# Performance work log

Measured on AMD Instinct MI355X. Metric: run time of the kernel, lower is better.

## Reference

```python
import jax, jax.numpy as jnp
import numpy as np

B, L, D, H, E, M, P = 2, 512, 768, 12, 32, 4, 256
EMB, BS, MAP, C = 768, 64, 256, 97


def setup_inputs() -> dict:
    key = jax.random.key(0)
    ks = jax.random.split(key, 16)
    w = lambda k, s: (0.02 * jax.random.normal(k, s, jnp.float32))
    seq = jax.random.normal(ks[0], (B, L, D), jnp.float32)
    attn = jax.random.uniform(ks[1], (B, H, L, L), jnp.float32)
    entity_pos = jax.random.randint(ks[2], (B, E, M), 0, L - 2)
    # distinct (h, t) entity pairs per document -> unique mention-pair scatter slots
    grid = jnp.stack(jnp.meshgrid(jnp.arange(E), jnp.arange(E), indexing='ij'), -1).reshape(-1, 2)
    hts = jnp.stack([grid[jax.random.permutation(jax.random.fold_in(ks[3], b), E * E)[:P]] for b in range(B)], 0)
    mention_idx = jnp.broadcast_to(jnp.arange(E * M).reshape(E, M), (B, E, M))
    return {
        'seq': seq, 'attn': attn,
        'entity_pos': entity_pos, 'hts': hts, 'mention_idx': mention_idx,
        'W_head': w(ks[4], (2 * D, EMB)), 'b_head': jnp.zeros((EMB,), jnp.float32),
        'W_tail': w(ks[5], (2 * D, EMB)), 'b_tail': jnp.zeros((EMB,), jnp.float32),
        'W_rel': w(ks[6], (EMB * BS, C)), 'b_rel': jnp.zeros((C,), jnp.float32),
        'W_fh': w(ks[7], (D, EMB)), 'W_ft': w(ks[8], (D, EMB)), 'b_f': jnp.zeros((EMB,), jnp.float32),
        'W_unet': w(ks[9], (EMB, C)), 'b_unet': jnp.zeros((C,), jnp.float32),
        'W_mlp': w(ks[10], (EMB, C)), 'b_mlp': jnp.zeros((C,), jnp.float32),
        'W_bil': w(ks[11], (3 * C, C)), 'b_bil': jnp.zeros((C,), jnp.float32),
    }


def reference(seq, attn, entity_pos, hts, mention_idx,
              W_head, b_head, W_tail, b_tail, W_rel, b_rel,
              W_fh, W_ft, b_f, W_unet, b_unet, W_mlp, b_mlp, W_bil, b_bil):
    pos = entity_pos + 1                                 # bert offset
    b3 = jnp.arange(B)[:, None, None]
    ment_emb = seq[b3, pos]                              # [B,E,M,D] mention gather
    ment_att = attn[b3, :, pos]                          # [B,E,M,H,L]
    ent_emb = jax.nn.logsumexp(ment_emb, axis=2)         # [B,E,D] logsumexp pool
    ent_att = ment_att.mean(axis=2)                      # [B,E,H,L]
    b2 = jnp.arange(B)[:, None]
    h_idx, t_idx = hts[..., 0], hts[..., 1]
    hs, ts = ent_emb[b2, h_idx], ent_emb[b2, t_idx]      # [B,P,D]
    ha, ta = ent_att[b2, h_idx], ent_att[b2, t_idx]      # [B,P,H,L]
    ht_att = (ha * ta).mean(2)                           # [B,P,L]
    ht_att = ht_att / (ht_att.sum(-1, keepdims=True) + 1e-5)
    rs = jnp.einsum('bld,bpl->bpd', seq, ht_att)         # localized context
    N = B * P
    hz = jnp.tanh(jnp.concatenate([hs, rs], -1).reshape(N, 2 * D) @ W_head + b_head)
    tz = jnp.tanh(jnp.concatenate([ts, rs], -1).reshape(N, 2 * D) @ W_tail + b_tail)
    bl = (hz.reshape(N, EMB // BS, BS, 1) * tz.reshape(N, EMB // BS, 1, BS)).reshape(N, EMB * BS)
    r1 = bl @ W_rel + b_rel                              # [N,C]
    # mention-pair dense map scatter (map_rss)
    ment_flat = ment_emb.reshape(B, E * M, D)
    mh = mention_idx[b2, h_idx]                          # [B,P,M]
    mt = mention_idx[b2, t_idx]
    mh2 = jnp.broadcast_to(mh[:, :, :, None], (B, P, M, M))
    mt2 = jnp.broadcast_to(mt[:, :, None, :], (B, P, M, M))
    b4 = jnp.broadcast_to(jnp.arange(B)[:, None, None, None], (B, P, M, M))
    eh = ment_flat[b4, mh2]                              # [B,P,M,M,D]
    et = ment_flat[b4, mt2]
    feat = eh @ W_fh + et @ W_ft + b_f                   # fused Linear(cat(h,t))
    mp = jnp.zeros((B, MAP, MAP, EMB), seq.dtype).at[b4, mh2, mt2].set(feat)
    enc2 = jnp.tanh(mp @ W_unet + b_unet)                # UNet-channel surrogate
    enc3 = jax.nn.gelu(mp @ W_mlp + b_mlp)               # MLP-channel surrogate
    r2 = jax.nn.logsumexp(enc2[b4, mh2, mt2], axis=(2, 3)).reshape(N, C)
    r3 = jax.nn.logsumexp(enc3[b4, mh2, mt2], axis=(2, 3)).reshape(N, C)
    return jnp.concatenate([r1, r2, r3], -1) @ W_bil + b_bil
```

## Files before the change

### kernel.cpp

```cpp
#include <hip/hip_runtime.h>
#include <hip/hip_bf16.h>

#define B_  2
#define L_  512
#define D_  768
#define H_  12
#define E_  32
#define M_  4
#define P_  256
#define EMB_ 768
#define BS_ 64
#define C_  97
#define N_  (B_*P_)

#define KTOT_    49152
#define CPAD_    112
#define KSPLIT_  48
#define KCHUNK_  (KTOT_/KSPLIT_)
#define PSTR_    128
#define TILE_    (CPAD_*64)

typedef __hip_bfloat16 bf16;
typedef __attribute__((ext_vector_type(8))) short bf16x8;
typedef __attribute__((ext_vector_type(4))) float f32x4;
typedef __attribute__((ext_vector_type(8))) float f32x8;

__device__ inline float ldIn(const void* p, long idx, int isbf) {
    return isbf ? (float)((const bf16*)p)[idx] : ((const float*)p)[idx];
}

__device__ inline unsigned short f2bf(float f) {
    bf16 h = (bf16)f;
    return *(unsigned short*)&h;
}

__device__ inline float bf2f(unsigned short u) {
    bf16 h = *(bf16*)&u;
    return (float)h;
}

__global__ void dtype_detect(const void* __restrict__ seq, int* __restrict__ flag,
                             float* __restrict__ c23) {
    __shared__ int cnt;
    if (threadIdx.x == 0) cnt = 0;
    if (threadIdx.x < 2*C_) c23[threadIdx.x] = 0.f;
    __syncthreads();
    const unsigned short* u = (const unsigned short*)seq;
    int bad = 0;
    for (int i = threadIdx.x; i < 1024; i += 256) {
        unsigned short e = (u[i] >> 7) & 0xFF;
        if (e >= 140) bad++;
    }
    atomicAdd(&cnt, bad);
    __syncthreads();
    if (threadIdx.x == 0) flag[0] = (cnt < 16) ? 1 : 0;
}

struct PrepArgs {
    const void* src[8];
    long off[8];
    int K[8];
    int Ncols[8];
    int Npad[8];
    unsigned short* dst[8];
    const void* W_bil;  float* W_bilF;
    const void* b_f; const void* W_unet; const void* b_unet;
    const void* W_mlp; const void* b_mlp; float* c23;
    const void* W_rel; unsigned short* WBt;
};

union PrepSm {
    float T[32][65];
    unsigned short TW[CPAD_][72];
};

__global__ void prep_kernel(PrepArgs a, const int* __restrict__ dtf) {
    int isbf = dtf[0];
    int z = blockIdx.z;
    __shared__ PrepSm sm;
    int tid = threadIdx.x;
    if (z == 0) {
        int lin = blockIdx.y*48 + blockIdx.x;
        if (lin >= 96) return;
        int c = tid;
        if (c >= C_) return;
        float s2 = 0.f, s3 = 0.f;
        int d0 = lin*8;
        for (int i = 0; i < 8; i++) {
            int d = d0 + i;
            float bf = ldIn(a.b_f, d, isbf);
            s2 += bf * ldIn(a.W_unet, (long)d*C_ + c, isbf);
            s3 += bf * ldIn(a.W_mlp,  (long)d*C_ + c, isbf);
        }
        if (lin == 0) {
            s2 += ldIn(a.b_unet, c, isbf);
            s3 += ldIn(a.b_mlp,  c, isbf);
        }
        atomicAdd(&a.c23[c], s2);
        atomicAdd(&a.c23[C_ + c], s3);
    } else if (z == 1) {
        int lin = blockIdx.y*48 + blockIdx.x;
        if (lin >= KTOT_/64) return;
        int k0 = lin * 64;
        for (int idx = tid; idx < 64*97; idx += 256) {
            int kk = idx / 97, c = idx % 97;
            sm.TW[c][kk] = f2bf(ldIn(a.W_rel, (long)(k0+kk)*C_ + c, isbf));
        }
        for (int idx = tid; idx < 15*64; idx += 256) {
            sm.TW[97 + (idx>>6)][idx & 63] = 0;
        }
        __syncthreads();
        unsigned short* tb = a.WBt + (long)lin*TILE_;
        for (int t = 0; t < 4; t++) {
            int idx = tid + t*256;
            if (idx < 896) {
                int c = idx >> 3, kc = idx & 7;
                *(uint4*)(tb + idx*8) = *(uint4*)&sm.TW[c][kc*8];
            }
        }
    } else if (z <= 9) {
        int j = z - 2;
        int K = a.K[j], Ncols = a.Ncols[j], Npad = a.Npad[j];
        int k0 = blockIdx.x*32, n0 = blockIdx.y*64;
        if (k0 >= K || n0 >= Npad) return;
        const void* src = a.src[j];
        long off = a.off[j];
        unsigned short* dst = a.dst[j];
        int c64 = tid & 63, r4 = tid >> 6;
        for (int p = 0; p < 8; p++) {
            int r = r4 + p*4;
            int n = n0 + c64;
            sm.T[r][c64] = (n < Ncols) ? ldIn(src, off + (long)(k0+r)*Ncols + n, isbf) : 0.f;
        }
        __syncthreads();
        int cc = tid & 31, n8 = tid >> 5;
        for (int p = 0; p < 8; p++) {
            int nn = n8 + p*8;
            dst[(long)(n0+nn)*K + k0 + cc] = f2bf(sm.T[cc][nn]);
        }
    } else {
        int lin = blockIdx.y*48 + blockIdx.x;
        int idx = lin*256 + tid;
        if (idx < 291*C_) a.W_bilF[idx] = ldIn(a.W_bil, idx, isbf);
    }
}

__global__ void gather_kernel(const void* __restrict__ seq, const void* __restrict__ attn,
                              const int* __restrict__ entity_pos,
                              unsigned short* __restrict__ mentb, float* __restrict__ ent_emb,
                              float* __restrict__ ent_att, const int* __restrict__ dtf) {
    int isbf = dtf[0];
    if (blockIdx.x < 768) {
        int beh = blockIdx.x;
        int h = beh % H_;
        int be = beh / H_;
        int b = be >> 5;
        int pos[M_];
        for (int m = 0; m < M_; m++) pos[m] = entity_pos[be*M_+m] + 1;
        for (int l = threadIdx.x; l < L_; l += 256) {
            float s = 0.f;
            for (int m = 0; m < M_; m++)
                s += ldIn(attn, (((long)(b*H_ + h))*L_ + pos[m])*L_ + l, isbf);
            ent_att[(long)beh*L_ + l] = 0.25f * s;
        }
    } else {
        int be = blockIdx.x - 768;
        int b = be >> 5;
        int pos[M_];
        for (int m = 0; m < M_; m++) pos[m] = entity_pos[be*M_+m] + 1;
        for (int d = threadIdx.x; d < D_; d += 256) {
            float x[M_];
            for (int m = 0; m < M_; m++) {
                x[m] = ldIn(seq, ((long)b*L_ + pos[m])*D_ + d, isbf);
                mentb[((long)be*M_ + m)*D_ + d] = f2bf(x[m]);
            }
            float mx = fmaxf(fmaxf(x[0],x[1]), fmaxf(x[2],x[3]));
            float s = expf(x[0]-mx)+expf(x[1]-mx)+expf(x[2]-mx)+expf(x[3]-mx);
            ent_emb[(long)be*D_ + d] = mx + logf(s);
        }
    }
}

__global__ void htatt_kernel(const float* __restrict__ ent_att, const int* __restrict__ hts,
                             unsigned short* __restrict__ htb) {
    int bp = blockIdx.x;
    int b = bp >> 8;
    int h_e = hts[bp*2+0], t_e = hts[bp*2+1];
    const float* ea_h = ent_att + (long)((b*E_ + h_e)*H_)*L_;
    const float* ea_t = ent_att + (long)((b*E_ + t_e)*H_)*L_;
    __shared__ float red[256];
    float v[2];
    for (int t = 0; t < 2; t++) {
        int l = threadIdx.x + t*256;
        float s = 0.f;
        for (int h = 0; h < H_; h++) s += ea_h[h*L_+l] * ea_t[h*L_+l];
        v[t] = s * (1.0f/H_);
    }
    red[threadIdx.x] = v[0] + v[1];
    __syncthreads();
    for (int off = 128; off > 0; off >>= 1) {
        if (threadIdx.x < off) red[threadIdx.x] += red[threadIdx.x+off];
        __syncthreads();
    }
    float inv = 1.0f / (red[0] + 1e-5f);
    for (int t = 0; t < 2; t++) {
        int l = threadIdx.x + t*256;
        htb[(long)bp*L_ + l] = f2bf(v[t] * inv);
    }
}

__global__ void catb_kernel(const float* __restrict__ ent_emb, const float* __restrict__ rs,
                            const int* __restrict__ hts,
                            unsigned short* __restrict__ hcatb, unsigned short* __restrict__ tcatb) {
    int n = blockIdx.x;
    int b = n >> 8;
    int h_e = hts[n*2+0], t_e = hts[n*2+1];
    const float* eh = ent_emb + (long)(b*E_ + h_e)*D_;
    const float* et = ent_emb + (long)(b*E_ + t_e)*D_;
    const float* r  = rs + (long)n*D_;
    for (int k = threadIdx.x; k < D_; k += 256) {
        hcatb[(long)n*1536 + k] = f2bf(eh[k]);
        tcatb[(long)n*1536 + k] = f2bf(et[k]);
        unsigned short rb = f2bf(r[k]);
        hcatb[(long)n*1536 + 768 + k] = rb;
        tcatb[(long)n*1536 + 768 + k] = rb;
    }
}

struct MfmaJob {
    const unsigned short* A[4];
    const unsigned short* Bt[4];
    const void* bias[4];
    void* C[4];
    int K[4];
    int ldc[4];
    int act[4];
    int obf[4];
};

__global__ void mfma_nt2_kernel(MfmaJob args, const int* __restrict__ dtf) {
    int z = blockIdx.z;
    const unsigned short* A  = args.A[z];
    const unsigned short* Bt = args.Bt[z];
    const void* bias = args.bias[z];
    void* C = args.C[z];
    int K = args.K[z], ldc = args.ldc[z], act = args.act[z], obf = args.obf[z];
    __shared__ unsigned short Al[2][32][72];
    __shared__ unsigned short Btl[2][32][72];
    int m0 = blockIdx.x*32, n0 = blockIdx.y*32;
    int tid = threadIdx.x, wave = tid>>6, lane = tid&63;
    int lm = lane&15, lq = lane>>4;
    int rowg = wave>>1, cgrp = wave&1;
    int rr = tid >> 3;
    int kc = (tid & 7) * 8;
    uint4 ra, rb;

    ra = *(const uint4*)(A  + (long)(m0+rr)*K + kc);
    rb = *(const uint4*)(Bt + (long)(n0+rr)*K + kc);
    *(uint4*)&Al[0][rr][kc]  = ra;
    *(uint4*)&Btl[0][rr][kc] = rb;

    int nst = K >> 6;
    f32x4 acc = {};
    for (int ks = 0; ks < nst; ks++) {
        __syncthreads();
        if (ks+1 < nst) {
            int k0 = (ks+1) << 6;
            ra = *(const uint4*)(A  + (long)(m0+rr)*K + k0 + kc);
            rb = *(const uint4*)(Bt + (long)(n0+rr)*K + k0 + kc);
        }
        int cb = ks & 1;
        #pragma unroll
        for (int half = 0; half < 2; half++) {
            bf16x8 af  = *(bf16x8*)&Al[cb][rowg*16+lm][half*32+lq*8];
            bf16x8 bfr = *(bf16x8*)&Btl[cb][cgrp*16+lm][half*32+lq*8];
            acc = __builtin_amdgcn_mfma_f32_16x16x32_bf16(af, bfr, acc, 0, 0, 0);
        }
        if (ks+1 < nst) {
            int nb = (ks+1) & 1;
            *(uint4*)&Al[nb][rr][kc]  = ra;
            *(uint4*)&Btl[nb][rr][kc] = rb;
        }
    }
    int isbf = dtf[0];
    int n = n0 + cgrp*16 + lm;
    float bia = bias ? ldIn(bias, n, isbf) : 0.f;
    #pragma unroll
    for (int r = 0; r < 4; r++) {
        int m = m0 + rowg*16 + lq*4 + r;
        float v = acc[r] + bia;
        if (act == 1) v = tanhf(v);
        if (obf) ((unsigned short*)C)[(long)m*ldc + n] = f2bf(v);
        else     ((float*)C)[(long)m*ldc + n] = v;
    }
}

__global__ __launch_bounds__(512, 4)
void r1_mfma_kernel(const float* __restrict__ hz, const float* __restrict__ tz,
                    const unsigned short* __restrict__ WBt,
                    float* __restrict__ partial) {
    __shared__ unsigned short Btl[2][CPAD_][72];
    __shared__ float hzL[64][17];
    int kz = blockIdx.x;
    int nb0 = blockIdx.y * 64;
    int gk0 = kz * (KCHUNK_/64);
    int gi0 = kz * 16;
    int g0 = (kz * KCHUNK_) >> 12;
    int tid = threadIdx.x;
    int wave = tid >> 6, lane = tid & 63;
    int lm = lane & 15, lq = lane >> 4;
    int rowg = wave >> 1;
    int cgrp = wave & 1;
    int nct = 4 - cgrp;
    int nrow = nb0 + rowg*16 + lm;

    {
        int r = tid >> 3, q = (tid & 7) * 2;
        float2 v = *(const float2*)(hz + (long)(nb0 + r)*EMB_ + gi0 + q);
        hzL[r][q] = v.x; hzL[r][q+1] = v.y;
    }
    f32x8 t0, t1;
    {
        const float* tp = tz + (long)nrow*EMB_ + g0*64;
        float4 x0 = *(const float4*)(tp + lq*8);
        float4 y0 = *(const float4*)(tp + lq*8 + 4);
        float4 x1 = *(const float4*)(tp + 32 + lq*8);
        float4 y1 = *(const float4*)(tp + 32 + lq*8 + 4);
        t0[0]=x0.x; t0[1]=x0.y; t0[2]=x0.z; t0[3]=x0.w;
        t0[4]=y0.x; t0[5]=y0.y; t0[6]=y0.z; t0[7]=y0.w;
        t1[0]=x1.x; t1[1]=x1.y; t1[2]=x1.z; t1[3]=x1.w;
        t1[4]=y1.x; t1[5]=y1.y; t1[6]=y1.z; t1[7]=y1.w;
    }

    {
        const unsigned short* tbp = WBt + (long)gk0*TILE_;
        #pragma unroll
        for (int t = 0; t < 2; t++) {
            int idx = tid + t*512;
            if (idx < 896) {
                *(uint4*)&Btl[0][idx>>3][(idx&7)*8] = *(const uint4*)(tbp + idx*8);
            }
        }
    }

    f32x4 acc[4] = {};
    uint4 rb[2];
    #pragma unroll 2
    for (int ks = 0; ks < KCHUNK_/64; ks++) {
        __syncthreads();
        if (ks+1 < KCHUNK_/64) {
            const unsigned short* tbp = WBt + (long)(gk0+ks+1)*TILE_;
            #pragma unroll
            for (int t = 0; t < 2; t++) {
                int idx = tid + t*512;
                if (idx < 896) {
                    rb[t] = *(const uint4*)(tbp + idx*8);
                }
            }
        }
        int cb = ks & 1;
        bf16x8 bf0[4], bf1[4];
        #pragma unroll
        for (int ct = 0; ct < 4; ct++) {
            if (ct < nct) {
                bf0[ct] = *(bf16x8*)&Btl[cb][(cgrp*4+ct)*16 + lm][lq*8];
                bf1[ct] = *(bf16x8*)&Btl[cb][(cgrp*4+ct)*16 + lm][32 + lq*8];
            }
        }
        float hvk = hzL[rowg*16 + lm][ks];
        unsigned short oa0[8], oa1[8];
        #pragma unroll
        for (int e = 0; e < 8; e++) {
            oa0[e] = f2bf(t0[e] * hvk);
            oa1[e] = f2bf(t1[e] * hvk);
        }
        bf16x8 a0 = *(bf16x8*)oa0;
        bf16x8 a1 = *(bf16x8*)oa1;
        #pragma unroll
        for (int ct = 0; ct < 4; ct++) {
            if (ct < nct) {
                acc[ct] = __builtin_amdgcn_mfma_f32_16x16x32_bf16(a0, bf0[ct], acc[ct], 0, 0, 0);
                acc[ct] = __builtin_amdgcn_mfma_f32_16x16x32_bf16(a1, bf1[ct], acc[ct], 0, 0, 0);
            }
        }
        if (ks+1 < KCHUNK_/64) {
            int nb = (ks+1) & 1;
            #pragma unroll
            for (int t = 0; t < 2; t++) {
                int idx = tid + t*512;
                if (idx < 896) {
                    *(uint4*)&Btl[nb][idx>>3][(idx&7)*8] = rb[t];
                }
            }
        }
    }
    #pragma unroll
    for (int ct = 0; ct < 4; ct++) {
        int c = (cgrp*4 + ct)*16 + lm;
        #pragma unroll
        for (int r = 0; r < 4; r++) {
            int nl = rowg*16 + lq*4 + r;
            partial[((long)(nb0+nl)*KSPLIT_ + kz)*PSTR_ + c] = acc[ct][r];
        }
    }
}

__global__ void r23out_kernel(const float* __restrict__ partial, const void* __restrict__ b_rel,
                              const float* __restrict__ mu, const float* __restrict__ c23,
                              const int* __restrict__ hts, const int* __restrict__ mention_idx,
                              const float* __restrict__ W_bilF, const void* __restrict__ b_bil,
                              void* __restrict__ out, const int* __restrict__ dtf) {
    int bp = blockIdx.x;
    int b = bp >> 8;
    int c = threadIdx.x;
    int isbf = dtf[0];
    __shared__ float row[292];
    if (c < C_) {
        const float* pr = partial + (long)bp*KSPLIT_*PSTR_;
        float r1v = 0.f;
        #pragma unroll 8
        for (int kz = 0; kz < KSPLIT_; kz++)
            r1v += pr[kz*PSTR_ + c];
        r1v += ldIn(b_rel, c, isbf);
        int h_e = hts[bp*2+0], t_e = hts[bp*2+1];
        const float* mu2h = mu;
        const float* mu2t = mu + 32768;
        const float* mu3h = mu + 65536;
        const float* mu3t = mu + 98304;
        float ah2[4], at2[4], ah3[4], at3[4];
        for (int m = 0; m < 4; m++) {
            int emh = mention_idx[(b*E_ + h_e)*M_ + m];
            int emt = mention_idx[(b*E_ + t_e)*M_ + m];
            ah2[m] = mu2h[(long)(b*128 + emh)*128 + c];
            ah3[m] = mu3h[(long)(b*128 + emh)*128 + c];
            at2[m] = mu2t[(long)(b*128 + emt)*128 + c];
            at3[m] = mu3t[(long)(b*128 + emt)*128 + c];
        }
        float c2 = c23[c], c3 = c23[C_ + c];
        float v2[16], v3[16];
        int q = 0;
        for (int i = 0; i < 4; i++) {
            for (int j = 0; j < 4; j++, q++) {
                float x2 = ah2[i] + at2[j] + c2;
                v2[q] = tanhf(x2);
                float x3 = ah3[i] + at3[j] + c3;
                float t = tanhf(0.7978845608028654f * (x3 + 0.044715f*x3*x3*x3));
                v3[q] = 0.5f * x3 * (1.0f + t);
            }
        }
        float m2 = v2[0], m3 = v3[0];
        for (q = 1; q < 16; q++) { m2 = fmaxf(m2, v2[q]); m3 = fmaxf(m3, v3[q]); }
        float s2 = 0.f, s3 = 0.f;
        for (q = 0; q < 16; q++) { s2 += expf(v2[q]-m2); s3 += expf(v3[q]-m3); }
        row[c]        = r1v;
        row[C_ + c]   = m2 + logf(s2);
        row[2*C_ + c] = m3 + logf(s3);
    }
    __syncthreads();
    if (c >= C_) return;
    float a0 = 0.f, a1 = 0.f, a2 = 0.f, a3 = 0.f;
    #pragma unroll 4
    for (int k = 0; k < 288; k += 4) {
        a0 += row[k+0] * W_bilF[(k+0)*C_ + c];
        a1 += row[k+1] * W_bilF[(k+1)*C_ + c];
        a2 += row[k+2] * W_bilF[(k+2)*C_ + c];
        a3 += row[k+3] * W_bilF[(k+3)*C_ + c];
    }
    a0 += row[288] * W_bilF[288*C_ + c];
    a1 += row[289] * W_bilF[289*C_ + c];
    a2 += row[290] * W_bilF[290*C_ + c];
    float v = a0 + a1 + a2 + a3 + ldIn(b_bil, c, isbf);
    if (isbf) ((bf16*)out)[(long)bp*C_ + c] = (bf16)v;
    else      ((float*)out)[(long)bp*C_ + c] = v;
}

extern "C" void kernel_launch(void* const* d_in, const int* in_sizes, int n_in,
                              void* d_out, int out_size, void* d_ws, size_t ws_size,
                              hipStream_t stream) {
    const void* seq        = d_in[0];
    const void* attn       = d_in[1];
    const int*  entity_pos = (const int*)d_in[2];
    const int*  hts        = (const int*)d_in[3];
    const int*  mention_idx= (const int*)d_in[4];
    const void* W_head     = d_in[5];
    const void* b_head     = d_in[6];
    const void* W_tail     = d_in[7];
    const void* b_tail     = d_in[8];
    const void* W_rel      = d_in[9];
    const void* b_rel      = d_in[10];
    const void* W_fh       = d_in[11];
    const void* W_ft       = d_in[12];
    const void* b_f        = d_in[13];
    const void* W_unet     = d_in[14];
    const void* b_unet     = d_in[15];
    const void* W_mlp      = d_in[16];
    const void* b_mlp      = d_in[17];
    const void* W_bil      = d_in[18];
    const void* b_bil      = d_in[19];

    float* w = (float*)d_ws;
    int*   dtf      = (int*)w;
    unsigned short* mentb = (unsigned short*)(w + 64);
    float* ent_emb  = w + 98368;
    float* ent_att  = w + 147520;
    unsigned short* htb = (unsigned short*)(w + 540736);
    float* rs       = w + 671808;
    float* hz       = w + 1065024;
    float* tz       = w + 1458240;
    float* mu       = w + 1851456;
    float* c23      = w + 1982528;
    unsigned short* seqT  = (unsigned short*)(w + 1982784);
    unsigned short* WhT   = (unsigned short*)(w + 2376000);
    unsigned short* WtT   = (unsigned short*)(w + 2965824);
    unsigned short* WfhT  = (unsigned short*)(w + 3555648);
    unsigned short* WftT  = (unsigned short*)(w + 3850560);
    unsigned short* WunetT= (unsigned short*)(w + 4145472);
    unsigned short* WmlpT = (unsigned short*)(w + 4194624);
    unsigned short* Tbh   = (unsigned short*)(w + 4243776);
    unsigned short* Tbt   = (unsigned short*)(w + 4342080);
    unsigned short* hcatb = (unsigned short*)(w + 4440384);
    unsigned short* tcatb = (unsigned short*)(w + 4833600);
    unsigned short* WBt   = (unsigned short*)(w + 5226816);
    float* partial  = w + 7979328;
    float* W_bilF   = w + 11649344;

    dtype_detect<<<1, 256, 0, stream>>>(seq, dtf, c23);
    {
        PrepArgs a = {};
        const void* srcs[8] = {W_head, W_tail, W_fh, W_ft, W_unet, W_mlp, seq, seq};
        long offs[8]   = {0,0,0,0,0,0,0,393216};
        int Ks[8]      = {1536,1536,768,768,768,768,512,512};
        int Ncols8[8]  = {768,768,768,768,97,97,768,768};
        int Npads[8]   = {768,768,768,768,128,128,768,768};
        unsigned short* dsts[8] = {WhT, WtT, WfhT, WftT, WunetT, WmlpT, seqT, seqT+393216};
        for (int z = 0; z < 8; z++) {
            a.src[z]=srcs[z]; a.off[z]=offs[z]; a.K[z]=Ks[z];
            a.Ncols[z]=Ncols8[z]; a.Npad[z]=Npads[z]; a.dst[z]=dsts[z];
        }
        a.W_bil = W_bil; a.W_bilF = W_bilF;
        a.b_f = b_f; a.W_unet = W_unet; a.b_unet = b_unet;
        a.W_mlp = W_mlp; a.b_mlp = b_mlp; a.c23 = c23;
        a.W_rel = W_rel; a.WBt = WBt;
        prep_kernel<<<dim3(48, 16, 11), 256, 0, stream>>>(a, dtf);
    }
    gather_kernel<<<768 + 64, 256, 0, stream>>>(seq, attn, entity_pos, mentb, ent_emb, ent_att, dtf);
    htatt_kernel<<<N_, 256, 0, stream>>>(ent_att, hts, htb);
    {
        MfmaJob ga = {};
        for (int z = 0; z < 2; z++) {
            ga.A[z] = htb + (long)z*256*512; ga.Bt[z] = seqT + (long)z*393216;
            ga.bias[z] = nullptr; ga.C[z] = rs + (long)z*256*768;
            ga.K[z] = 512; ga.ldc[z] = 768; ga.act[z] = 0; ga.obf[z] = 0;
        }
        ga.A[2] = mentb; ga.Bt[2] = WfhT; ga.bias[2] = nullptr; ga.C[2] = Tbh;
        ga.K[2] = 768; ga.ldc[2] = 768; ga.act[2] = 0; ga.obf[2] = 1;
        ga.A[3] = mentb; ga.Bt[3] = WftT; ga.bias[3] = nullptr; ga.C[3] = Tbt;
        ga.K[3] = 768; ga.ldc[3] = 768; ga.act[3] = 0; ga.obf[3] = 1;
        mfma_nt2_kernel<<<dim3(8, 24, 4), 256, 0, stream>>>(ga, dtf);
    }
    catb_kernel<<<N_, 256, 0, stream>>>(ent_emb, rs, hts, hcatb, tcatb);
    {
        MfmaJob ga = {};
        ga.A[0] = hcatb; ga.Bt[0] = WhT; ga.bias[0] = b_head; ga.C[0] = hz;
        ga.A[1] = tcatb; ga.Bt[1] = WtT; ga.bias[1] = b_tail; ga.C[1] = tz;
        for (int z = 0; z < 2; z++) { ga.K[z] = 1536; ga.ldc[z] = 768; ga.act[z] = 1; ga.obf[z] = 0; }
        mfma_nt2_kernel<<<dim3(16, 24, 2), 256, 0, stream>>>(ga, dtf);
    }
    {
        MfmaJob ga = {};
        const unsigned short* As[4] = {Tbh, Tbt, Tbh, Tbt};
        const unsigned short* Bs[4] = {WunetT, WunetT, WmlpT, WmlpT};
        for (int q = 0; q < 4; q++) {
            ga.A[q] = As[q]; ga.Bt[q] = Bs[q]; ga.bias[q] = nullptr;
            ga.C[q] = mu + q*32768;
            ga.K[q] = 768; ga.ldc[q] = 128; ga.act[q] = 0; ga.obf[q] = 0;
        }
        mfma_nt2_kernel<<<dim3(8, 4, 4), 256, 0, stream>>>(ga, dtf);
    }
    r1_mfma_kernel<<<dim3(KSPLIT_, 8), 512, 0, stream>>>(hz, tz, WBt, partial);
    r23out_kernel<<<N_, 128, 0, stream>>>(partial, b_rel, mu, c23, hts, mention_idx,
                                          W_bilF, b_bil, d_out, dtf);
}
```

Baseline: 242.8 us.

## Load r1 weight tiles directly into registers and halve r1 block size

The r1 kernel no longer stages the bf16 W_rel tiles through double-buffered shared memory. Each wave now loads its MFMA B fragments straight from global memory into registers, with register-level prefetch of the next k-step. This removes the per-iteration barriers and the LDS writes and reads. Blocks shrink to 256 threads covering 32 rows, so the grid doubles. The trade-off is more global and L2 traffic, since each wave and each row block fetches the weights independently.

```diff
diff --git a/kernel.cpp b/kernel.cpp
--- a/kernel.cpp
+++ b/kernel.cpp
@@ -295,15 +295,14 @@
     }
 }
 
-__global__ __launch_bounds__(512, 4)
+__global__ __launch_bounds__(256, 3)
 void r1_mfma_kernel(const float* __restrict__ hz, const float* __restrict__ tz,
                     const unsigned short* __restrict__ WBt,
                     float* __restrict__ partial) {
-    __shared__ unsigned short Btl[2][CPAD_][72];
-    __shared__ float hzL[64][17];
+    __shared__ float hzL[32][17];
     int kz = blockIdx.x;
-    int nb0 = blockIdx.y * 64;
-    int gk0 = kz * (KCHUNK_/64);
+    int nb0 = blockIdx.y * 32;
+    int gk0 = kz * 16;
     int gi0 = kz * 16;
     int g0 = (kz * KCHUNK_) >> 12;
     int tid = threadIdx.x;
@@ -331,40 +330,30 @@
         t1[0]=x1.x; t1[1]=x1.y; t1[2]=x1.z; t1[3]=x1.w;
         t1[4]=y1.x; t1[5]=y1.y; t1[6]=y1.z; t1[7]=y1.w;
     }
-
-    {
-        const unsigned short* tbp = WBt + (long)gk0*TILE_;
-        #pragma unroll
-        for (int t = 0; t < 2; t++) {
-            int idx = tid + t*512;
-            if (idx < 896) {
-                *(uint4*)&Btl[0][idx>>3][(idx&7)*8] = *(const uint4*)(tbp + idx*8);
-            }
-        }
-    }
+    __syncthreads();
+
+    const unsigned short* wb = WBt + (long)gk0*TILE_ + (cgrp*64 + lm)*64 + lq*8;
 
     f32x4 acc[4] = {};
-    uint4 rb[2];
+    bf16x8 cb0[4], cb1[4];
+    #pragma unroll
+    for (int ct = 0; ct < 4; ct++) {
+        if (ct < nct) {
+            cb0[ct] = *(const bf16x8*)(wb + ct*1024);
+            cb1[ct] = *(const bf16x8*)(wb + ct*1024 + 32);
+        }
+    }
     #pragma unroll 2
     for (int ks = 0; ks < KCHUNK_/64; ks++) {
-        __syncthreads();
+        bf16x8 nb0r[4], nb1r[4];
         if (ks+1 < KCHUNK_/64) {
-            const unsigned short* tbp = WBt + (long)(gk0+ks+1)*TILE_;
+            const unsigned short* wn = wb + (long)(ks+1)*TILE_;
             #pragma unroll
-            for (int t = 0; t < 2; t++) {
-                int idx = tid + t*512;
-                if (idx < 896) {
-                    rb[t] = *(const uint4*)(tbp + idx*8);
+            for (int ct = 0; ct < 4; ct++) {
+                if (ct < nct) {
+                    nb0r[ct] = *(const bf16x8*)(wn + ct*1024);
+                    nb1r[ct] = *(const bf16x8*)(wn + ct*1024 + 32);
                 }
-            }
-        }
-        int cb = ks & 1;
-        bf16x8 bf0[4], bf1[4];
-        #pragma unroll
-        for (int ct = 0; ct < 4; ct++) {
-            if (ct < nct) {
-                bf0[ct] = *(bf16x8*)&Btl[cb][(cgrp*4+ct)*16 + lm][lq*8];
-                bf1[ct] = *(bf16x8*)&Btl[cb][(cgrp*4+ct)*16 + lm][32 + lq*8];
             }
         }
         float hvk = hzL[rowg*16 + lm][ks];
@@ -379,18 +368,14 @@
         #pragma unroll
         for (int ct = 0; ct < 4; ct++) {
             if (ct < nct) {
-                acc[ct] = __builtin_amdgcn_mfma_f32_16x16x32_bf16(a0, bf0[ct], acc[ct], 0, 0, 0);
-                acc[ct] = __builtin_amdgcn_mfma_f32_16x16x32_bf16(a1, bf1[ct], acc[ct], 0, 0, 0);
+                acc[ct] = __builtin_amdgcn_mfma_f32_16x16x32_bf16(a0, cb0[ct], acc[ct], 0, 0, 0);
+                acc[ct] = __builtin_amdgcn_mfma_f32_16x16x32_bf16(a1, cb1[ct], acc[ct], 0, 0, 0);
             }
         }
         if (ks+1 < KCHUNK_/64) {
-            int nb = (ks+1) & 1;
             #pragma unroll
-            for (int t = 0; t < 2; t++) {
-                int idx = tid + t*512;
-                if (idx < 896) {
-                    *(uint4*)&Btl[nb][idx>>3][(idx&7)*8] = rb[t];
-                }
+            for (int ct = 0; ct < 4; ct++) {
+                if (ct < nct) { cb0[ct] = nb0r[ct]; cb1[ct] = nb1r[ct]; }
             }
         }
     }
@@ -577,7 +562,7 @@
         }
         mfma_nt2_kernel<<<dim3(8, 4, 4), 256, 0, stream>>>(ga, dtf);
     }
-    r1_mfma_kernel<<<dim3(KSPLIT_, 8), 512, 0, stream>>>(hz, tz, WBt, partial);
+    r1_mfma_kernel<<<dim3(KSPLIT_, 16), 256, 0, stream>>>(hz, tz, WBt, partial);
     r23out_kernel<<<N_, 128, 0, stream>>>(partial, b_rel, mu, c23, hts, mention_idx,
                                           W_bilF, b_bil, d_out, dtf);
 }
```

Measured after the change: 244.0 us. Within noise of the previous version (+0.5%).
